# Optimization experiments

Measured on AMD Instinct MI355X. Metric: run time of the kernel, lower is better.

## Reference

```python
import jax, jax.numpy as jnp
import numpy as np
from jax import lax

# Constants matching PostProcess(conf_thres=0.4, iou_thres=0.5, merge=False, agnostic=False)
CONF_THRES = 0.4
IOU_THRES = 0.5
MAX_WH = 4096.0   # per-class box offset (agnostic=False)
MAX_DET = 300     # hardcoded in module
MAX_NMS = 30000   # cap on NMS candidates (yolov5 convention); JAX needs static shapes
B, N, NC = 16, 25200, 80


def setup_inputs() -> dict:
    key = jax.random.key(0)
    u = jax.random.uniform(key, (B, N, 5 + NC), dtype=jnp.float32)
    # cx,cy in [0,640); w,h in [2,102); obj and class scores in [0,1)
    scale = jnp.concatenate([jnp.array([640.0, 640.0, 100.0, 100.0], jnp.float32),
                             jnp.ones((1 + NC,), jnp.float32)])
    shift = jnp.concatenate([jnp.array([0.0, 0.0, 2.0, 2.0], jnp.float32),
                             jnp.zeros((1 + NC,), jnp.float32)])
    prediction = u * scale + shift
    return {"prediction": prediction}


def _cxcywh_to_xyxy(x):
    cx, cy, w, h = x[..., 0], x[..., 1], x[..., 2], x[..., 3]
    return jnp.stack([cx - 0.5 * w, cy - 0.5 * h, cx + 0.5 * w, cy + 0.5 * h], axis=-1)


def _process_one(x):  # x: [N, 5+NC]
    obj = x[:, 4]
    cls_conf = x[:, 5:] * obj[:, None]          # x[:,5:] *= x[:,4:5]
    box = _cxcywh_to_xyxy(x[:, :4])             # [N, 4]
    # multi-label candidate mask: obj > conf AND class conf > conf (x[xc] then x[:,5:] > conf)
    cand = (obj[:, None] > CONF_THRES) & (cls_conf > CONF_THRES)   # [N, NC]
    flat = jnp.where(cand, cls_conf, 0.0).reshape(-1)              # [N*NC]
    top_scores, top_idx = lax.top_k(flat, MAX_NMS)                 # static-size candidate set
    bi = top_idx // NC                                             # box index i
    cj = (top_idx % NC).astype(jnp.float32)                        # class index j
    cand_boxes = box[bi]                                           # [M, 4]
    scores0 = jnp.where(top_scores > CONF_THRES, top_scores, 0.0)  # 0 marks invalid/suppressed
    off_boxes = cand_boxes + cj[:, None] * MAX_WH                  # per-class offset for NMS
    areas = (off_boxes[:, 2] - off_boxes[:, 0]) * (off_boxes[:, 3] - off_boxes[:, 1])
    idx_range = jnp.arange(MAX_NMS)

    def step(scores, _):
        # greedy NMS: pick best remaining, suppress IoU > thresh (torchvision semantics)
        idx = jnp.argmax(scores)
        s = scores[idx]
        keep = s > 0.0
        b = off_boxes[idx]
        lt = jnp.maximum(b[:2], off_boxes[:, :2])
        rb = jnp.minimum(b[2:], off_boxes[:, 2:])
        wh = jnp.clip(rb - lt, 0.0)
        inter = wh[:, 0] * wh[:, 1]
        iou = inter / (areas[idx] + areas - inter + 1e-9)
        suppress = (iou > IOU_THRES) | (idx_range == idx)
        return jnp.where(suppress, 0.0, scores), (idx, keep)

    _, (keep_idx, keep_flag) = lax.scan(step, scores0, None, length=MAX_DET)
    rows = jnp.concatenate([cand_boxes[keep_idx],
                            top_scores[keep_idx][:, None],
                            cj[keep_idx][:, None]], axis=1)        # [MAX_DET, 6] = xyxy, conf, cls
    return jnp.where(keep_flag[:, None], rows, 0.0)


def reference(prediction):
    # Padded fixed-shape analogue of torch.stack(output): [B, MAX_DET, 6], zero rows = no detection
    return jax.vmap(_process_one)(prediction)
```

## Files before the change

### kernel.cpp

```cpp
#include <hip/hip_runtime.h>
#include <stdint.h>

#define BATCH 16
#define NROW 25200
#define NCLS 80
#define ROWF 85
#define MAXDET 300
#define MAXNMS 30000u
#define NBIN 3072
#define BASEBITS 0x3EC00000u
#define CAP 32768u
#define BATCH_FLOATS 2142000

#define PREBIN 2048
#define NBUCK 1024
#define CANDCAP 131072u
#define KMAX 2048u

#define GATHER_MIN 512u
#define SORTCAP 1024
#define CH_SZ 128

#define TILE_ROWS 80
#define TILE_FLOATS 6800
#define RPB 400
#define SUBT 5
#define SBLK 63

#define ROWS_PER_BLK 256
#define SBLK2 99

__device__ __forceinline__ bool iou_gt_half(float ax1, float ay1, float ax2, float ay2, float aa,
                                            float bx1, float by1, float bx2, float by2, float ba) {
    float ltx = fmaxf(ax1, bx1), lty = fmaxf(ay1, by1);
    float rbx = fminf(ax2, bx2), rby = fminf(ay2, by2);
    float wx = fmaxf(__fsub_rn(rbx, ltx), 0.0f);
    float wy = fmaxf(__fsub_rn(rby, lty), 0.0f);
    float inter = __fmul_rn(wx, wy);
    float den = __fadd_rn(__fsub_rn(__fadd_rn(aa, ba), inter), 1e-9f);
    float t = __fmul_rn(0.5f, den);
    if (!(inter > t)) return false;
    float tg = __fmul_rn(0.50000012f, den);
    if (inter >= tg) return true;
    return __fdiv_rn(inter, den) > 0.5f;
}

__device__ __forceinline__ unsigned bin_of_bits(unsigned bits) {
    unsigned v = (bits - BASEBITS) >> 12;
    if (v > (unsigned)(NBIN - 1)) v = NBIN - 1;
    return v;
}

__global__ __launch_bounds__(256) void k_stage(const float* __restrict__ pred,
                                               unsigned* __restrict__ ghist,
                                               unsigned* __restrict__ ccnt,
                                               unsigned long long* __restrict__ cand,
                                               unsigned* __restrict__ oflow,
                                               int staged) {
    if (!staged) return;
    __shared__ unsigned shist[NBUCK];
    __shared__ unsigned long long skey[KMAX];
    __shared__ unsigned s_cnt, s_n, s_base;
    int bx = blockIdx.x;
    int b = bx / SBLK2, blk = bx - b * SBLK2;
    int t = threadIdx.x, lane = t & 63, wv = t >> 6;
    for (int i = t; i < NBUCK; i += 256) shist[i] = 0u;
    if (t == 0) s_cnt = 0u;
    __syncthreads();
    const float* pb = pred + (size_t)b * BATCH_FLOATS;
    int r0 = blk * ROWS_PER_BLK + wv * 64;
    int rown = NROW - r0;
    if (rown > 0) {
        if (rown > 64) rown = 64;
        float obj = 0.0f;
        if (lane < rown) obj = pb[(size_t)(r0 + lane) * ROWF + 4];
        unsigned long long live = __ballot(obj > 0.4f);
        while (live) {
            int j = (int)__builtin_ctzll(live);
            live &= live - 1ULL;
            float o = __shfl(obj, j);
            const float* rp = pb + (size_t)(r0 + j) * ROWF;
            unsigned grow = (unsigned)(r0 + j);
            {
                float s = __fmul_rn(rp[5 + lane], o);
                if (s >= 0.75f) {
                    unsigned bits = __float_as_uint(s);
                    unsigned bin = bin_of_bits(bits);
                    atomicAdd(&shist[bin - PREBIN], 1u);
                    unsigned u = atomicAdd(&s_cnt, 1u);
                    unsigned flat = grow * (unsigned)NCLS + (unsigned)lane;
                    if (u < KMAX)
                        skey[u] = ((unsigned long long)bits << 32) |
                                  (unsigned long long)(0xFFFFFFFFu - flat);
                    else oflow[b] = 1u;
                }
            }
            if (lane < 16) {
                int c = 64 + lane;
                float s = __fmul_rn(rp[5 + c], o);
                if (s >= 0.75f) {
                    unsigned bits = __float_as_uint(s);
                    unsigned bin = bin_of_bits(bits);
                    atomicAdd(&shist[bin - PREBIN], 1u);
                    unsigned u = atomicAdd(&s_cnt, 1u);
                    unsigned flat = grow * (unsigned)NCLS + (unsigned)c;
                    if (u < KMAX)
                        skey[u] = ((unsigned long long)bits << 32) |
                                  (unsigned long long)(0xFFFFFFFFu - flat);
                    else oflow[b] = 1u;
                }
            }
        }
    }
    __syncthreads();
    unsigned* gh = ghist + (size_t)(b * SBLK2 + blk) * NBUCK;
    for (int i = t; i < NBUCK; i += 256) gh[i] = shist[i];
    if (t == 0) {
        unsigned n = s_cnt;
        if (n > KMAX) n = KMAX;
        unsigned base = atomicAdd(&ccnt[b], n);
        if (base + n > CANDCAP) oflow[b] = 1u;
        s_n = n; s_base = base;
    }
    __syncthreads();
    unsigned n = s_n, base = s_base;
    if (base + n <= CANDCAP) {
        unsigned long long* cd = cand + (size_t)b * CANDCAP + base;
        for (unsigned k = t; k < n; k += 256) cd[k] = skey[k];
    }
}

__global__ __launch_bounds__(256) void k_prep(const unsigned* __restrict__ ghist,
                                              const unsigned* __restrict__ ccnt,
                                              const unsigned* __restrict__ oflow,
                                              unsigned* __restrict__ suf2,
                                              int* __restrict__ meta,
                                              int staged) {
    __shared__ unsigned sh[NBUCK];
    __shared__ unsigned sS[NBUCK];
    __shared__ unsigned cs[256];
    __shared__ int s_cut, s_need, s_tot;
    __shared__ unsigned s_bad;
    int b = blockIdx.x, t = threadIdx.x;
    for (int i = t; i < NBUCK; i += 256) {
        unsigned s = 0;
        const unsigned* g = ghist + (size_t)b * SBLK2 * NBUCK + i;
        for (int k = 0; k < SBLK2; ++k) s += g[(size_t)k * NBUCK];
        sh[i] = s;
    }
    if (t == 0) { s_cut = -1; s_need = 0; s_tot = 0; s_bad = 0u; }
    __syncthreads();
    for (int i = t; i < NBUCK; i += 256)
        if (sh[i] > (unsigned)SORTCAP) atomicOr(&s_bad, 1u);
    const int CHUNK = NBUCK / 256;
    int base = t * CHUNK;
    unsigned tot = 0;
    for (int i = 0; i < CHUNK; ++i) tot += sh[base + i];
    cs[t] = tot;
    __syncthreads();
    for (int off = 1; off < 256; off <<= 1) {
        unsigned v = (t + off < 256) ? cs[t + off] : 0u;
        __syncthreads();
        cs[t] += v;
        __syncthreads();
    }
    unsigned after = (t + 1 < 256) ? cs[t + 1] : 0u;
    for (int i = CHUNK - 1; i >= 0; --i) {
        after += sh[base + i];
        sS[base + i] = after;
    }
    __syncthreads();
    unsigned* g2 = suf2 + (size_t)b * (NBUCK + 1);
    for (int i = t; i < NBUCK; i += 256) g2[i] = sS[i];
    if (t == 0) g2[NBUCK] = 0u;
    for (int i = 0; i < CHUNK; ++i) {
        int v = base + i;
        unsigned Sv = sS[v];
        unsigned Sn = (v + 1 < NBUCK) ? sS[v + 1] : 0u;
        if (Sv >= MAXNMS && Sn < MAXNMS) {
            s_cut = PREBIN + v;
            s_need = (int)(MAXNMS - Sn);
            s_tot = (int)Sv;
        }
    }
    __syncthreads();
    if (t == 0) {
        int valid = (staged && s_cut >= 0 && s_bad == 0u &&
                     oflow[b] == 0u && ccnt[b] <= CANDCAP) ? 1 : 0;
        meta[b * 4 + 0] = valid ? s_cut : 0;
        meta[b * 4 + 1] = valid ? s_need : 0;
        meta[b * 4 + 2] = valid ? s_tot : 0;
        meta[b * 4 + 3] = valid;
    }
}

__global__ __launch_bounds__(256) void k_hist_fb(const float* __restrict__ pred,
                                                 unsigned* __restrict__ hist,
                                                 const int* __restrict__ meta) {
    int bx = blockIdx.x;
    int b = bx / SBLK, blk = bx - b * SBLK;
    if (meta[b * 4 + 3]) return;
    __shared__ __align__(16) float rows[TILE_FLOATS];
    __shared__ unsigned shist[NBIN];
    int t = threadIdx.x, lane = t & 63, wv = t >> 6;
    for (int i = t; i < NBIN; i += 256) shist[i] = 0u;
    const float* pbase = pred + (size_t)b * BATCH_FLOATS + (size_t)blk * RPB * ROWF;
    for (int st = 0; st < SUBT; ++st) {
        __syncthreads();
        const float4* src = (const float4*)(pbase + (size_t)st * TILE_ROWS * ROWF);
        float4* dst = (float4*)rows;
        for (int i = t; i < TILE_FLOATS / 4; i += 256) dst[i] = src[i];
        __syncthreads();
        for (int r = wv; r < TILE_ROWS; r += 4) {
            float obj = rows[r * ROWF + 4];
            if (!(obj > 0.4f)) continue;
            for (int half = 0; half < 2; ++half) {
                int c = lane + (half << 6);
                if (c < NCLS) {
                    float cv = rows[r * ROWF + 5 + c];
                    float s = __fmul_rn(cv, obj);
                    if (s > 0.4f) atomicAdd(&shist[bin_of_bits(__float_as_uint(s))], 1u);
                }
            }
        }
    }
    __syncthreads();
    unsigned* gh = hist + (size_t)b * NBIN;
    for (int i = t; i < NBIN; i += 256) {
        unsigned v = shist[i];
        if (v) atomicAdd(&gh[i], v);
    }
}

__global__ __launch_bounds__(256) void k_scan_fb(const unsigned* __restrict__ hist,
                                                 unsigned* __restrict__ suf,
                                                 int* __restrict__ meta) {
    int b = blockIdx.x, t = threadIdx.x;
    if (meta[b * 4 + 3]) return;
    __shared__ unsigned sh[NBIN];
    __shared__ unsigned sS[NBIN];
    __shared__ unsigned cs[256];
    __shared__ int s_cut, s_need, s_tot;
    const unsigned* gh = hist + (size_t)b * NBIN;
    for (int i = t; i < NBIN; i += 256) sh[i] = gh[i];
    if (t == 0) { s_cut = 0; s_need = 0x7FFFFFFF; s_tot = 0; }
    __syncthreads();
    const int CHUNK = NBIN / 256;
    int base = t * CHUNK;
    unsigned tot = 0;
    for (int i = 0; i < CHUNK; ++i) tot += sh[base + i];
    cs[t] = tot;
    __syncthreads();
    for (int off = 1; off < 256; off <<= 1) {
        unsigned v = (t + off < 256) ? cs[t + off] : 0u;
        __syncthreads();
        cs[t] += v;
        __syncthreads();
    }
    unsigned after = (t + 1 < 256) ? cs[t + 1] : 0u;
    for (int i = CHUNK - 1; i >= 0; --i) {
        after += sh[base + i];
        sS[base + i] = after;
    }
    __syncthreads();
    unsigned* gs = suf + (size_t)b * (NBIN + 1);
    for (int i = t; i < NBIN; i += 256) gs[i] = sS[i];
    if (t == 0) gs[NBIN] = 0u;
    for (int i = 0; i < CHUNK; ++i) {
        int v = base + i;
        unsigned Sv = sS[v];
        unsigned Sn = (v + 1 < NBIN) ? sS[v + 1] : 0u;
        if (Sv >= MAXNMS && Sn < MAXNMS) {
            s_cut = v;
            s_need = (int)(MAXNMS - Sn);
            s_tot = (int)Sv;
        }
    }
    __syncthreads();
    if (t == 0) {
        int cut = s_cut, needv = s_need, totv = s_tot;
        if (sS[0] < MAXNMS) { cut = 0; needv = 0x7FFFFFFF; totv = (int)sS[0]; }
        meta[b * 4 + 0] = cut;
        meta[b * 4 + 1] = needv;
        meta[b * 4 + 2] = totv;
    }
}

__global__ __launch_bounds__(256) void k_scatter_fb(const float* __restrict__ pred,
                                                    const unsigned* __restrict__ suf,
                                                    const int* __restrict__ meta,
                                                    unsigned* __restrict__ cursor,
                                                    unsigned long long* __restrict__ keys) {
    int bx = blockIdx.x;
    int b = bx / SBLK, blk = bx - b * SBLK;
    if (meta[b * 4 + 3]) return;
    __shared__ __align__(16) float rows[TILE_FLOATS];
    int t = threadIdx.x, lane = t & 63, wv = t >> 6;
    int cutbin = meta[b * 4 + 0];
    const float* pbase = pred + (size_t)b * BATCH_FLOATS + (size_t)blk * RPB * ROWF;
    unsigned rowbase0 = (unsigned)(blk * RPB);
    const unsigned* gs = suf + (size_t)b * (NBIN + 1);
    unsigned* cur = cursor + (size_t)b * NBIN;
    unsigned long long* kb = keys + (size_t)b * CAP;
    for (int st = 0; st < SUBT; ++st) {
        __syncthreads();
        const float4* src = (const float4*)(pbase + (size_t)st * TILE_ROWS * ROWF);
        float4* dst = (float4*)rows;
        for (int i = t; i < TILE_FLOATS / 4; i += 256) dst[i] = src[i];
        __syncthreads();
        for (int r = wv; r < TILE_ROWS; r += 4) {
            float obj = rows[r * ROWF + 4];
            if (!(obj > 0.4f)) continue;
            unsigned grow = rowbase0 + (unsigned)(st * TILE_ROWS + r);
            for (int half = 0; half < 2; ++half) {
                int c = lane + (half << 6);
                if (c < NCLS) {
                    float cv = rows[r * ROWF + 5 + c];
                    float s = __fmul_rn(cv, obj);
                    if (s > 0.4f) {
                        unsigned bits = __float_as_uint(s);
                        unsigned bin = bin_of_bits(bits);
                        if ((int)bin >= cutbin) {
                            unsigned pos = gs[bin + 1] + atomicAdd(&cur[bin], 1u);
                            if (pos < CAP) {
                                unsigned flat = grow * (unsigned)NCLS + (unsigned)c;
                                kb[pos] = ((unsigned long long)bits << 32) |
                                          (unsigned long long)(0xFFFFFFFFu - flat);
                            }
                        }
                    }
                }
            }
        }
    }
}

__global__ __launch_bounds__(1024) void k_nms(const float* __restrict__ pred,
                                              const unsigned* __restrict__ suf,
                                              const unsigned* __restrict__ suf2,
                                              const int* __restrict__ meta,
                                              const unsigned* __restrict__ ccnt,
                                              const unsigned long long* __restrict__ keys,
                                              const unsigned long long* __restrict__ cand,
                                              float* __restrict__ out) {
    __shared__ unsigned sgsL[NBUCK + 1];
    __shared__ unsigned long long ktmp[SORTCAP];
    __shared__ unsigned long long skeys[SORTCAP];
    __shared__ unsigned maskW[CH_SZ][5];
    __shared__ unsigned sup0w[4];
    __shared__ float cbox[CH_SZ][9];
    __shared__ float kept[MAXDET][5];
    __shared__ int klist[MAXDET];
    __shared__ int s_nk, s_localk;
    __shared__ unsigned s_gc;

    int b = blockIdx.x;
    int tid = threadIdx.x;
    int lane = tid & 63, wv = tid >> 6;

    int cutbin = meta[b * 4 + 0];
    int needv  = meta[b * 4 + 1];
    unsigned total = (unsigned)meta[b * 4 + 2];
    int valid  = meta[b * 4 + 3];
    if (!valid && total > CAP) total = CAP;
    const unsigned* gs = suf + (size_t)b * (NBIN + 1);
    const unsigned* g2 = suf2 + (size_t)b * (NBUCK + 1);
    const unsigned long long* kb = keys + (size_t)b * CAP;
    const unsigned long long* cd = cand + (size_t)b * CANDCAP;
    unsigned ccb = valid ? ccnt[b] : 0u;
    if (ccb > CANDCAP) ccb = CANDCAP;
    const float* pb = pred + (size_t)b * BATCH_FLOATS;
    float* ob = out + (size_t)b * MAXDET * 6;

    if (valid) for (int i = tid; i < NBUCK + 1; i += 1024) sgsL[i] = g2[i];
    if (tid == 0) s_nk = 0;
    __syncthreads();

#define GSV(v) (valid ? sgsL[(v) - PREBIN] : gs[(v)])

    unsigned limit;
    if (needv == 0x7FFFFFFF) limit = total;
    else limit = GSV(cutbin + 1) + (unsigned)needv;
    if (limit > total) limit = total;

    unsigned p = 0;
    while (p < limit) {
        if (s_nk >= MAXDET) break;

        int lo = cutbin, hi = NBIN - 1, w1 = cutbin;
        while (lo <= hi) { int mid = (lo + hi) >> 1;
            if (GSV(mid) > p) { w1 = mid; lo = mid + 1; } else hi = mid - 1; }
        lo = cutbin; hi = NBIN - 1; int w2 = cutbin;
        while (lo <= hi) { int mid = (lo + hi) >> 1;
            if (GSV(mid) >= p + GATHER_MIN) { w2 = mid; lo = mid + 1; } else hi = mid - 1; }
        unsigned gEnd = GSV(w2);
        if (gEnd <= p) gEnd = GSV(cutbin);
        if (gEnd - p > (unsigned)SORTCAP) {
            if (w2 < w1) gEnd = GSV(w2 + 1);
            if (gEnd - p > (unsigned)SORTCAP) gEnd = p + SORTCAP;
        }
        unsigned G = gEnd - p;

        if (valid) {
            if (tid == 0) s_gc = 0u;
            __syncthreads();
            for (unsigned k = tid; k < ccb; k += 1024) {
                unsigned long long key = cd[k];
                unsigned v = bin_of_bits((unsigned)(key >> 32));
                if ((int)v >= w2 && (int)v <= w1) {
                    unsigned u = atomicAdd(&s_gc, 1u);
                    if (u < (unsigned)SORTCAP) ktmp[u] = key;
                }
            }
            __syncthreads();
            unsigned Gc = s_gc; if (Gc > (unsigned)SORTCAP) Gc = (unsigned)SORTCAP;
            if (tid < (int)Gc) {
                unsigned long long key = ktmp[tid];
                unsigned v = bin_of_bits((unsigned)(key >> 32));
                unsigned bstart = GSV(v + 1);
                unsigned rank = 0;
                for (unsigned u = 0; u < Gc; ++u) {
                    unsigned long long kk = ktmp[u];
                    unsigned vu = bin_of_bits((unsigned)(kk >> 32));
                    rank += (vu == v && kk > key) ? 1u : 0u;
                }
                skeys[(bstart - p) + rank] = key;
            }
            __syncthreads();
        } else {
            unsigned myLo = 0, myHi = 0;
            unsigned long long raw = 0ULL;
            if (tid < (int)G) {
                unsigned idx = p + (unsigned)tid;
                int l2 = cutbin, h2 = NBIN - 1, v = cutbin;
                while (l2 <= h2) { int mid = (l2 + h2) >> 1;
                    if (GSV(mid) > idx) { v = mid; l2 = mid + 1; } else h2 = mid - 1; }
                unsigned bstart = GSV(v + 1);
                unsigned bend = GSV(v);
                raw = kb[idx];
                myLo = bstart - p;
                myHi = bend - p; if (myHi > G) myHi = G;
                ktmp[tid] = raw;
            }
            __syncthreads();
            if (tid < (int)G) {
                unsigned rank = 0;
                for (unsigned u = myLo; u < myHi; ++u) rank += (ktmp[u] > raw) ? 1u : 0u;
                skeys[myLo + rank] = raw;
            }
            __syncthreads();
        }

        unsigned consumable = limit - p; if (consumable > G) consumable = G;

        for (unsigned c0 = 0; c0 < consumable; c0 += CH_SZ) {
            int nk0 = s_nk;
            if (nk0 >= MAXDET) break;
            int CH = (int)((consumable - c0 < (unsigned)CH_SZ) ? (consumable - c0) : (unsigned)CH_SZ);

            if (tid < CH_SZ * 5) maskW[tid / 5][tid % 5] = 0u;
            if (tid >= CH_SZ * 5 && tid < CH_SZ * 5 + 4) sup0w[tid - CH_SZ * 5] = 0u;
            if (tid < CH) {
                unsigned long long kk = skeys[c0 + tid];
                unsigned flat = 0xFFFFFFFFu - (unsigned)kk;
                unsigned bi = flat / (unsigned)NCLS;
                unsigned cc = flat - bi * (unsigned)NCLS;
                const float* rp = pb + (size_t)bi * ROWF;
                float cx = rp[0], cy = rp[1], wd = rp[2], ht = rp[3];
                float hw = __fmul_rn(0.5f, wd), hh = __fmul_rn(0.5f, ht);
                float off = __fmul_rn((float)cc, 4096.0f);
                float x1 = __fsub_rn(cx, hw), y1 = __fsub_rn(cy, hh);
                float x2 = __fadd_rn(cx, hw), y2 = __fadd_rn(cy, hh);
                float ox1 = __fadd_rn(x1, off), oy1 = __fadd_rn(y1, off);
                float ox2 = __fadd_rn(x2, off), oy2 = __fadd_rn(y2, off);
                cbox[tid][0] = ox1; cbox[tid][1] = oy1;
                cbox[tid][2] = ox2; cbox[tid][3] = oy2;
                cbox[tid][4] = __fmul_rn(__fsub_rn(ox2, ox1), __fsub_rn(oy2, oy1));
            }
            __syncthreads();

            {
                int col = tid & (CH_SZ - 1);
                int part = tid >> 7;
                if (col < CH) {
                    float bx1 = cbox[col][0], by1 = cbox[col][1];
                    float bx2 = cbox[col][2], by2 = cbox[col][3], ba = cbox[col][4];
                    unsigned part16 = 0u;
                    int rbase = part << 4;
                    for (int k = 0; k < 16; ++k) {
                        int i2 = rbase + k;
                        if (i2 >= col || i2 >= CH) break;
                        if (iou_gt_half(cbox[i2][0], cbox[i2][1], cbox[i2][2], cbox[i2][3],
                                        cbox[i2][4], bx1, by1, bx2, by2, ba))
                            part16 |= (1u << k);
                    }
                    if (part16)
                        atomicOr(&maskW[col][part >> 1], part16 << ((part & 1) << 4));
                    bool f = false;
                    for (int k2 = part; k2 < nk0; k2 += 8) {
                        if (iou_gt_half(kept[k2][0], kept[k2][1], kept[k2][2], kept[k2][3],
                                        kept[k2][4], bx1, by1, bx2, by2, ba)) f = true;
                    }
                    if (f) atomicOr(&sup0w[col >> 5], 1u << (col & 31));
                }
            }
            __syncthreads();

            if (wv == 0) {
                unsigned keptw = 0u;
                int nkv = nk0, lk = 0;
                unsigned pre0 = (lane < 4 && CH > 0) ? maskW[0][lane] : 0u;
                unsigned pre1 = (lane < 4 && CH > 1) ? maskW[1][lane] : 0u;
                for (int j = 0; j < CH && nkv < MAXDET; ++j) {
                    unsigned colw = pre0;
                    pre0 = pre1;
                    pre1 = (lane < 4 && (j + 2) < CH) ? maskW[j + 2][lane] : 0u;
                    bool hit = (keptw & colw) != 0u;
                    bool sup = __any(hit);
                    if ((sup0w[j >> 5] >> (j & 31)) & 1u) sup = true;
                    if (!sup) {
                        if (lane == (j >> 5)) keptw |= 1u << (j & 31);
                        if (lane == 0) klist[lk] = j;
                        lk++; nkv++;
                    }
                }
                if (lane == 0) { s_localk = lk; s_nk = nkv; }
            }
            __syncthreads();

            int lk = s_localk;
            for (int t2 = tid; t2 < lk; t2 += 1024) {
                int i = klist[t2];
                int oidx = nk0 + t2;
                kept[oidx][0] = cbox[i][0]; kept[oidx][1] = cbox[i][1];
                kept[oidx][2] = cbox[i][2]; kept[oidx][3] = cbox[i][3];
                kept[oidx][4] = cbox[i][4];
                unsigned long long kk = skeys[c0 + i];
                unsigned bits = (unsigned)(kk >> 32);
                unsigned flat = 0xFFFFFFFFu - (unsigned)kk;
                unsigned bi = flat / (unsigned)NCLS;
                unsigned cc = flat - bi * (unsigned)NCLS;
                const float* rp = pb + (size_t)bi * ROWF;
                float cx = rp[0], cy = rp[1], wd = rp[2], ht = rp[3];
                float hw = __fmul_rn(0.5f, wd), hh = __fmul_rn(0.5f, ht);
                float* orow = ob + (size_t)oidx * 6;
                orow[0] = __fsub_rn(cx, hw);
                orow[1] = __fsub_rn(cy, hh);
                orow[2] = __fadd_rn(cx, hw);
                orow[3] = __fadd_rn(cy, hh);
                orow[4] = __uint_as_float(bits);
                orow[5] = (float)cc;
            }
            __syncthreads();
        }
        p = gEnd;
    }
#undef GSV
}

extern "C" void kernel_launch(void* const* d_in, const int* in_sizes, int n_in,
                              void* d_out, int out_size, void* d_ws, size_t ws_size,
                              hipStream_t stream) {
    const float* pred = (const float*)d_in[0];
    float* outp = (float*)d_out;
    char* ws = (char*)d_ws;

    const size_t OFF_HIST = 0;
    const size_t SZ_HIST  = (size_t)BATCH * NBIN * 4;
    const size_t OFF_CUR  = OFF_HIST + SZ_HIST;
    const size_t SZ_CUR   = (size_t)BATCH * NBIN * 4;
    const size_t OFF_CCNT = OFF_CUR + SZ_CUR;
    const size_t SZ_CCNT  = (size_t)BATCH * 4;
    const size_t OFF_OFLW = OFF_CCNT + SZ_CCNT;
    const size_t SZ_OFLW  = (size_t)BATCH * 4;
    const size_t OFF_META = OFF_OFLW + SZ_OFLW;
    const size_t SZ_META  = (size_t)BATCH * 4 * 4;
    const size_t ZERO_SZ  = OFF_META + SZ_META;
    const size_t OFF_SUF  = ZERO_SZ;
    const size_t SZ_SUF   = (size_t)BATCH * (NBIN + 1) * 4;
    const size_t OFF_SUF2 = OFF_SUF + SZ_SUF;
    const size_t SZ_SUF2  = (size_t)BATCH * (NBUCK + 1) * 4;
    const size_t OFF_KEYS = OFF_SUF2 + SZ_SUF2;
    const size_t SZ_KEYS  = (size_t)BATCH * CAP * 8;
    const size_t OFF_GH   = OFF_KEYS + SZ_KEYS;
    const size_t SZ_GH    = (size_t)BATCH * SBLK2 * NBUCK * 4;
    const size_t OFF_CAND = OFF_GH + SZ_GH;
    const size_t SZ_CAND  = (size_t)BATCH * CANDCAP * 8;
    const size_t WS_NEEDED = OFF_CAND + SZ_CAND;

    int staged = (ws_size >= WS_NEEDED) ? 1 : 0;

    unsigned* hist             = (unsigned*)(ws + OFF_HIST);
    unsigned* cursor           = (unsigned*)(ws + OFF_CUR);
    unsigned* ccnt             = (unsigned*)(ws + OFF_CCNT);
    unsigned* oflow            = (unsigned*)(ws + OFF_OFLW);
    int* meta                  = (int*)(ws + OFF_META);
    unsigned* suf              = (unsigned*)(ws + OFF_SUF);
    unsigned* suf2             = (unsigned*)(ws + OFF_SUF2);
    unsigned long long* keys   = (unsigned long long*)(ws + OFF_KEYS);
    unsigned* ghist            = (unsigned*)(ws + OFF_GH);
    unsigned long long* cand   = (unsigned long long*)(ws + OFF_CAND);

    hipMemsetAsync(ws, 0, ZERO_SZ, stream);
    hipMemsetAsync(d_out, 0, (size_t)out_size * sizeof(float), stream);

    k_stage<<<dim3(BATCH * SBLK2), dim3(256), 0, stream>>>(pred, ghist, ccnt, cand, oflow, staged);
    k_prep<<<dim3(BATCH), dim3(256), 0, stream>>>(ghist, ccnt, oflow, suf2, meta, staged);
    k_hist_fb<<<dim3(BATCH * SBLK), dim3(256), 0, stream>>>(pred, hist, meta);
    k_scan_fb<<<dim3(BATCH), dim3(256), 0, stream>>>(hist, suf, meta);
    k_scatter_fb<<<dim3(BATCH * SBLK), dim3(256), 0, stream>>>(pred, suf, meta, cursor, keys);
    k_nms<<<dim3(BATCH), dim3(1024), 0, stream>>>(pred, suf, suf2, meta, ccnt, keys, cand, outp);
}
```

Measured before the change: 375.2 us.

## Pre-scatter top candidates into bucket-sorted buffer in prep kernel

The per-block histogram write is replaced by global atomic accumulation into one histogram per batch. The prep kernel now runs with 1024 threads, scans that histogram directly, finds a threshold bin covering the top 2048 candidates, and counting-scatters those candidates into a bucket-ordered keys2 buffer. The NMS kernel then reads its first phase from keys2 with in-bucket rank sorting, so it no longer rescans the whole candidate list for every gather chunk. The costs are global atomics in k_stage and a serial-per-batch scatter pass in k_prep.

```diff
diff --git a/kernel.cpp b/kernel.cpp
--- a/kernel.cpp
+++ b/kernel.cpp
@@ -16,8 +16,9 @@
 #define NBUCK 1024
 #define CANDCAP 131072u
 #define KMAX 2048u
-
-#define GATHER_MIN 512u
+#define TOPK 2048u
+#define K2CAP 4096u
+
 #define SORTCAP 1024
 #define CH_SZ 128
 
@@ -52,7 +53,7 @@
 }
 
 __global__ __launch_bounds__(256) void k_stage(const float* __restrict__ pred,
-                                               unsigned* __restrict__ ghist,
+                                               unsigned* __restrict__ hist2,
                                                unsigned* __restrict__ ccnt,
                                                unsigned long long* __restrict__ cand,
                                                unsigned* __restrict__ oflow,
@@ -113,8 +114,11 @@
         }
     }
     __syncthreads();
-    unsigned* gh = ghist + (size_t)(b * SBLK2 + blk) * NBUCK;
-    for (int i = t; i < NBUCK; i += 256) gh[i] = shist[i];
+    unsigned* gh = hist2 + (size_t)b * NBUCK;
+    for (int i = t; i < NBUCK; i += 256) {
+        unsigned v = shist[i];
+        if (v) atomicAdd(&gh[i], v);
+    }
     if (t == 0) {
         unsigned n = s_cnt;
         if (n > KMAX) n = KMAX;
@@ -130,67 +134,66 @@
     }
 }
 
-__global__ __launch_bounds__(256) void k_prep(const unsigned* __restrict__ ghist,
-                                              const unsigned* __restrict__ ccnt,
-                                              const unsigned* __restrict__ oflow,
-                                              unsigned* __restrict__ suf2,
-                                              int* __restrict__ meta,
-                                              int staged) {
-    __shared__ unsigned sh[NBUCK];
+__global__ __launch_bounds__(1024) void k_prep(const unsigned* __restrict__ hist2,
+                                               const unsigned* __restrict__ ccnt,
+                                               const unsigned* __restrict__ oflow,
+                                               const unsigned long long* __restrict__ cand,
+                                               unsigned* __restrict__ suf2,
+                                               unsigned long long* __restrict__ keys2,
+                                               int* __restrict__ meta,
+                                               int staged) {
     __shared__ unsigned sS[NBUCK];
-    __shared__ unsigned cs[256];
-    __shared__ int s_cut, s_need, s_tot;
-    __shared__ unsigned s_bad;
+    __shared__ unsigned scur[NBUCK];
+    __shared__ int s_cut, s_need, s_tot, s_T, s_valid;
+    __shared__ unsigned s_bad, s_E;
     int b = blockIdx.x, t = threadIdx.x;
-    for (int i = t; i < NBUCK; i += 256) {
-        unsigned s = 0;
-        const unsigned* g = ghist + (size_t)b * SBLK2 * NBUCK + i;
-        for (int k = 0; k < SBLK2; ++k) s += g[(size_t)k * NBUCK];
-        sh[i] = s;
-    }
-    if (t == 0) { s_cut = -1; s_need = 0; s_tot = 0; s_bad = 0u; }
-    __syncthreads();
-    for (int i = t; i < NBUCK; i += 256)
-        if (sh[i] > (unsigned)SORTCAP) atomicOr(&s_bad, 1u);
-    const int CHUNK = NBUCK / 256;
-    int base = t * CHUNK;
-    unsigned tot = 0;
-    for (int i = 0; i < CHUNK; ++i) tot += sh[base + i];
-    cs[t] = tot;
-    __syncthreads();
-    for (int off = 1; off < 256; off <<= 1) {
-        unsigned v = (t + off < 256) ? cs[t + off] : 0u;
-        __syncthreads();
-        cs[t] += v;
-        __syncthreads();
-    }
-    unsigned after = (t + 1 < 256) ? cs[t + 1] : 0u;
-    for (int i = CHUNK - 1; i >= 0; --i) {
-        after += sh[base + i];
-        sS[base + i] = after;
-    }
-    __syncthreads();
+    unsigned h = hist2[(size_t)b * NBUCK + t];
+    sS[t] = h;
+    if (t == 0) { s_cut = -1; s_T = -1; s_bad = 0u; s_need = 0; s_tot = 0; s_E = 0u; }
+    __syncthreads();
+    if (h > (unsigned)SORTCAP) atomicOr(&s_bad, 1u);
+    for (int off = 1; off < NBUCK; off <<= 1) {
+        unsigned v = (t + off < NBUCK) ? sS[t + off] : 0u;
+        __syncthreads();
+        sS[t] += v;
+        __syncthreads();
+    }
+    unsigned Sv = sS[t];
+    unsigned Sn = (t + 1 < NBUCK) ? sS[t + 1] : 0u;
+    if (Sv >= MAXNMS && Sn < MAXNMS) {
+        s_cut = PREBIN + t; s_need = (int)(MAXNMS - Sn); s_tot = (int)Sv;
+    }
+    if (Sv >= TOPK && Sn < TOPK) { s_T = PREBIN + t; s_E = Sv; }
     unsigned* g2 = suf2 + (size_t)b * (NBUCK + 1);
-    for (int i = t; i < NBUCK; i += 256) g2[i] = sS[i];
+    g2[t] = Sv;
     if (t == 0) g2[NBUCK] = 0u;
-    for (int i = 0; i < CHUNK; ++i) {
-        int v = base + i;
-        unsigned Sv = sS[v];
-        unsigned Sn = (v + 1 < NBUCK) ? sS[v + 1] : 0u;
-        if (Sv >= MAXNMS && Sn < MAXNMS) {
-            s_cut = PREBIN + v;
-            s_need = (int)(MAXNMS - Sn);
-            s_tot = (int)Sv;
+    scur[t] = Sn;
+    __syncthreads();
+    if (t == 0) {
+        int valid = (staged && s_cut >= 0 && s_T >= 0 && s_bad == 0u &&
+                     oflow[b] == 0u && ccnt[b] <= CANDCAP) ? 1 : 0;
+        s_valid = valid;
+        meta[b * 8 + 0] = valid ? s_cut : 0;
+        meta[b * 8 + 1] = valid ? s_need : 0;
+        meta[b * 8 + 2] = valid ? s_tot : 0;
+        meta[b * 8 + 3] = valid;
+        meta[b * 8 + 4] = valid ? s_T : 0;
+        meta[b * 8 + 5] = valid ? (int)s_E : 0;
+    }
+    __syncthreads();
+    if (s_valid) {
+        int T = s_T;
+        unsigned ccb = ccnt[b];
+        const unsigned long long* cd = cand + (size_t)b * CANDCAP;
+        unsigned long long* k2 = keys2 + (size_t)b * K2CAP;
+        for (unsigned k = t; k < ccb; k += 1024) {
+            unsigned long long key = cd[k];
+            unsigned v = bin_of_bits((unsigned)(key >> 32));
+            if ((int)v >= T) {
+                unsigned pos = atomicAdd(&scur[v - PREBIN], 1u);
+                if (pos < K2CAP) k2[pos] = key;
+            }
         }
-    }
-    __syncthreads();
-    if (t == 0) {
-        int valid = (staged && s_cut >= 0 && s_bad == 0u &&
-                     oflow[b] == 0u && ccnt[b] <= CANDCAP) ? 1 : 0;
-        meta[b * 4 + 0] = valid ? s_cut : 0;
-        meta[b * 4 + 1] = valid ? s_need : 0;
-        meta[b * 4 + 2] = valid ? s_tot : 0;
-        meta[b * 4 + 3] = valid;
     }
 }
 
@@ -199,7 +202,7 @@
                                                  const int* __restrict__ meta) {
     int bx = blockIdx.x;
     int b = bx / SBLK, blk = bx - b * SBLK;
-    if (meta[b * 4 + 3]) return;
+    if (meta[b * 8 + 3]) return;
     __shared__ __align__(16) float rows[TILE_FLOATS];
     __shared__ unsigned shist[NBIN];
     int t = threadIdx.x, lane = t & 63, wv = t >> 6;
@@ -217,8 +220,7 @@
             for (int half = 0; half < 2; ++half) {
                 int c = lane + (half << 6);
                 if (c < NCLS) {
-                    float cv = rows[r * ROWF + 5 + c];
-                    float s = __fmul_rn(cv, obj);
+                    float s = __fmul_rn(rows[r * ROWF + 5 + c], obj);
                     if (s > 0.4f) atomicAdd(&shist[bin_of_bits(__float_as_uint(s))], 1u);
                 }
             }
@@ -236,7 +238,7 @@
                                                  unsigned* __restrict__ suf,
                                                  int* __restrict__ meta) {
     int b = blockIdx.x, t = threadIdx.x;
-    if (meta[b * 4 + 3]) return;
+    if (meta[b * 8 + 3]) return;
     __shared__ unsigned sh[NBIN];
     __shared__ unsigned sS[NBIN];
     __shared__ unsigned cs[256];
@@ -271,18 +273,16 @@
         unsigned Sv = sS[v];
         unsigned Sn = (v + 1 < NBIN) ? sS[v + 1] : 0u;
         if (Sv >= MAXNMS && Sn < MAXNMS) {
-            s_cut = v;
-            s_need = (int)(MAXNMS - Sn);
-            s_tot = (int)Sv;
+            s_cut = v; s_need = (int)(MAXNMS - Sn); s_tot = (int)Sv;
         }
     }
     __syncthreads();
     if (t == 0) {
         int cut = s_cut, needv = s_need, totv = s_tot;
         if (sS[0] < MAXNMS) { cut = 0; needv = 0x7FFFFFFF; totv = (int)sS[0]; }
-        meta[b * 4 + 0] = cut;
-        meta[b * 4 + 1] = needv;
-        meta[b * 4 + 2] = totv;
+        meta[b * 8 + 0] = cut;
+        meta[b * 8 + 1] = needv;
+        meta[b * 8 + 2] = totv;
     }
 }
 
@@ -293,10 +293,10 @@
                                                     unsigned long long* __restrict__ keys) {
     int bx = blockIdx.x;
     int b = bx / SBLK, blk = bx - b * SBLK;
-    if (meta[b * 4 + 3]) return;
+    if (meta[b * 8 + 3]) return;
     __shared__ __align__(16) float rows[TILE_FLOATS];
     int t = threadIdx.x, lane = t & 63, wv = t >> 6;
-    int cutbin = meta[b * 4 + 0];
+    int cutbin = meta[b * 8 + 0];
     const float* pbase = pred + (size_t)b * BATCH_FLOATS + (size_t)blk * RPB * ROWF;
     unsigned rowbase0 = (unsigned)(blk * RPB);
     const unsigned* gs = suf + (size_t)b * (NBIN + 1);
@@ -315,8 +315,7 @@
             for (int half = 0; half < 2; ++half) {
                 int c = lane + (half << 6);
                 if (c < NCLS) {
-                    float cv = rows[r * ROWF + 5 + c];
-                    float s = __fmul_rn(cv, obj);
+                    float s = __fmul_rn(rows[r * ROWF + 5 + c], obj);
                     if (s > 0.4f) {
                         unsigned bits = __float_as_uint(s);
                         unsigned bin = bin_of_bits(bits);
@@ -341,6 +340,7 @@
                                               const int* __restrict__ meta,
                                               const unsigned* __restrict__ ccnt,
                                               const unsigned long long* __restrict__ keys,
+                                              const unsigned long long* __restrict__ keys2,
                                               const unsigned long long* __restrict__ cand,
                                               float* __restrict__ out) {
     __shared__ unsigned sgsL[NBUCK + 1];
@@ -358,14 +358,17 @@
     int tid = threadIdx.x;
     int lane = tid & 63, wv = tid >> 6;
 
-    int cutbin = meta[b * 4 + 0];
-    int needv  = meta[b * 4 + 1];
-    unsigned total = (unsigned)meta[b * 4 + 2];
-    int valid  = meta[b * 4 + 3];
+    int cutbin = meta[b * 8 + 0];
+    int needv  = meta[b * 8 + 1];
+    unsigned total = (unsigned)meta[b * 8 + 2];
+    int valid  = meta[b * 8 + 3];
+    int Tbin   = meta[b * 8 + 4];
+    unsigned E = valid ? (unsigned)meta[b * 8 + 5] : 0u;
     if (!valid && total > CAP) total = CAP;
     const unsigned* gs = suf + (size_t)b * (NBIN + 1);
     const unsigned* g2 = suf2 + (size_t)b * (NBUCK + 1);
     const unsigned long long* kb = keys + (size_t)b * CAP;
+    const unsigned long long* k2 = keys2 + (size_t)b * K2CAP;
     const unsigned long long* cd = cand + (size_t)b * CANDCAP;
     unsigned ccb = valid ? ccnt[b] : 0u;
     if (ccb > CANDCAP) ccb = CANDCAP;
@@ -387,27 +390,49 @@
     while (p < limit) {
         if (s_nk >= MAXDET) break;
 
-        int lo = cutbin, hi = NBIN - 1, w1 = cutbin;
+        int lo = cutbin, hi = NBIN - 1, vs = NBIN - 1;
         while (lo <= hi) { int mid = (lo + hi) >> 1;
-            if (GSV(mid) > p) { w1 = mid; lo = mid + 1; } else hi = mid - 1; }
-        lo = cutbin; hi = NBIN - 1; int w2 = cutbin;
-        while (lo <= hi) { int mid = (lo + hi) >> 1;
-            if (GSV(mid) >= p + GATHER_MIN) { w2 = mid; lo = mid + 1; } else hi = mid - 1; }
-        unsigned gEnd = GSV(w2);
-        if (gEnd <= p) gEnd = GSV(cutbin);
-        if (gEnd - p > (unsigned)SORTCAP) {
-            if (w2 < w1) gEnd = GSV(w2 + 1);
-            if (gEnd - p > (unsigned)SORTCAP) gEnd = p + SORTCAP;
-        }
+            if (GSV(mid) <= p + (unsigned)SORTCAP) { vs = mid; hi = mid - 1; } else lo = mid + 1; }
+        unsigned gEnd = GSV(vs);
+        bool phaseA = (!valid) || (p < E);
+        if (valid && phaseA && gEnd > E) gEnd = E;
+        if (gEnd > total) gEnd = total;
+        if (gEnd <= p) { gEnd = p + (unsigned)SORTCAP; if (gEnd > total) gEnd = total; }
         unsigned G = gEnd - p;
 
-        if (valid) {
+        if (phaseA) {
+            const unsigned long long* src = valid ? k2 : kb;
+            unsigned myLo = 0, myHi = 0;
+            unsigned long long raw = 0ULL;
+            if (tid < (int)G) {
+                unsigned idx = p + (unsigned)tid;
+                int l2 = cutbin, h2 = NBIN - 1, v = cutbin;
+                while (l2 <= h2) { int mid = (l2 + h2) >> 1;
+                    if (GSV(mid) > idx) { v = mid; l2 = mid + 1; } else h2 = mid - 1; }
+                unsigned bstart = GSV(v + 1);
+                unsigned bend = GSV(v);
+                raw = src[idx];
+                myLo = (bstart > p) ? (bstart - p) : 0u;
+                myHi = bend - p; if (myHi > G) myHi = G;
+                ktmp[tid] = raw;
+            }
+            __syncthreads();
+            if (tid < (int)G) {
+                unsigned rank = 0;
+                for (unsigned u = myLo; u < myHi; ++u) rank += (ktmp[u] > raw) ? 1u : 0u;
+                skeys[myLo + rank] = raw;
+            }
+            __syncthreads();
+        } else {
+            int l0 = cutbin, h0 = NBIN - 1, w1 = cutbin;
+            while (l0 <= h0) { int mid = (l0 + h0) >> 1;
+                if (GSV(mid) > p) { w1 = mid; l0 = mid + 1; } else h0 = mid - 1; }
             if (tid == 0) s_gc = 0u;
             __syncthreads();
             for (unsigned k = tid; k < ccb; k += 1024) {
                 unsigned long long key = cd[k];
                 unsigned v = bin_of_bits((unsigned)(key >> 32));
-                if ((int)v >= w2 && (int)v <= w1) {
+                if ((int)v >= vs && (int)v <= w1) {
                     unsigned u = atomicAdd(&s_gc, 1u);
                     if (u < (unsigned)SORTCAP) ktmp[u] = key;
                 }
@@ -425,28 +450,6 @@
                     rank += (vu == v && kk > key) ? 1u : 0u;
                 }
                 skeys[(bstart - p) + rank] = key;
-            }
-            __syncthreads();
-        } else {
-            unsigned myLo = 0, myHi = 0;
-            unsigned long long raw = 0ULL;
-            if (tid < (int)G) {
-                unsigned idx = p + (unsigned)tid;
-                int l2 = cutbin, h2 = NBIN - 1, v = cutbin;
-                while (l2 <= h2) { int mid = (l2 + h2) >> 1;
-                    if (GSV(mid) > idx) { v = mid; l2 = mid + 1; } else h2 = mid - 1; }
-                unsigned bstart = GSV(v + 1);
-                unsigned bend = GSV(v);
-                raw = kb[idx];
-                myLo = bstart - p;
-                myHi = bend - p; if (myHi > G) myHi = G;
-                ktmp[tid] = raw;
-            }
-            __syncthreads();
-            if (tid < (int)G) {
-                unsigned rank = 0;
-                for (unsigned u = myLo; u < myHi; ++u) rank += (ktmp[u] > raw) ? 1u : 0u;
-                skeys[myLo + rank] = raw;
             }
             __syncthreads();
         }
@@ -565,49 +568,52 @@
     float* outp = (float*)d_out;
     char* ws = (char*)d_ws;
 
-    const size_t OFF_HIST = 0;
-    const size_t SZ_HIST  = (size_t)BATCH * NBIN * 4;
-    const size_t OFF_CUR  = OFF_HIST + SZ_HIST;
-    const size_t SZ_CUR   = (size_t)BATCH * NBIN * 4;
-    const size_t OFF_CCNT = OFF_CUR + SZ_CUR;
-    const size_t SZ_CCNT  = (size_t)BATCH * 4;
-    const size_t OFF_OFLW = OFF_CCNT + SZ_CCNT;
-    const size_t SZ_OFLW  = (size_t)BATCH * 4;
-    const size_t OFF_META = OFF_OFLW + SZ_OFLW;
-    const size_t SZ_META  = (size_t)BATCH * 4 * 4;
-    const size_t ZERO_SZ  = OFF_META + SZ_META;
-    const size_t OFF_SUF  = ZERO_SZ;
-    const size_t SZ_SUF   = (size_t)BATCH * (NBIN + 1) * 4;
-    const size_t OFF_SUF2 = OFF_SUF + SZ_SUF;
-    const size_t SZ_SUF2  = (size_t)BATCH * (NBUCK + 1) * 4;
-    const size_t OFF_KEYS = OFF_SUF2 + SZ_SUF2;
-    const size_t SZ_KEYS  = (size_t)BATCH * CAP * 8;
-    const size_t OFF_GH   = OFF_KEYS + SZ_KEYS;
-    const size_t SZ_GH    = (size_t)BATCH * SBLK2 * NBUCK * 4;
-    const size_t OFF_CAND = OFF_GH + SZ_GH;
-    const size_t SZ_CAND  = (size_t)BATCH * CANDCAP * 8;
+    const size_t OFF_HIST  = 0;
+    const size_t SZ_HIST   = (size_t)BATCH * NBIN * 4;
+    const size_t OFF_CUR   = OFF_HIST + SZ_HIST;
+    const size_t SZ_CUR    = (size_t)BATCH * NBIN * 4;
+    const size_t OFF_H2    = OFF_CUR + SZ_CUR;
+    const size_t SZ_H2     = (size_t)BATCH * NBUCK * 4;
+    const size_t OFF_CCNT  = OFF_H2 + SZ_H2;
+    const size_t SZ_CCNT   = (size_t)BATCH * 4;
+    const size_t OFF_OFLW  = OFF_CCNT + SZ_CCNT;
+    const size_t SZ_OFLW   = (size_t)BATCH * 4;
+    const size_t OFF_META  = OFF_OFLW + SZ_OFLW;
+    const size_t SZ_META   = (size_t)BATCH * 8 * 4;
+    const size_t ZERO_SZ   = OFF_META + SZ_META;
+    const size_t OFF_SUF   = ZERO_SZ;
+    const size_t SZ_SUF    = (size_t)BATCH * (NBIN + 1) * 4;
+    const size_t OFF_SUF2  = OFF_SUF + SZ_SUF;
+    const size_t SZ_SUF2   = (size_t)BATCH * (NBUCK + 1) * 4;
+    const size_t OFF_KEYS  = OFF_SUF2 + SZ_SUF2;
+    const size_t SZ_KEYS   = (size_t)BATCH * CAP * 8;
+    const size_t OFF_K2    = OFF_KEYS + SZ_KEYS;
+    const size_t SZ_K2     = (size_t)BATCH * K2CAP * 8;
+    const size_t OFF_CAND  = OFF_K2 + SZ_K2;
+    const size_t SZ_CAND   = (size_t)BATCH * CANDCAP * 8;
     const size_t WS_NEEDED = OFF_CAND + SZ_CAND;
 
     int staged = (ws_size >= WS_NEEDED) ? 1 : 0;
 
     unsigned* hist             = (unsigned*)(ws + OFF_HIST);
     unsigned* cursor           = (unsigned*)(ws + OFF_CUR);
+    unsigned* hist2            = (unsigned*)(ws + OFF_H2);
     unsigned* ccnt             = (unsigned*)(ws + OFF_CCNT);
     unsigned* oflow            = (unsigned*)(ws + OFF_OFLW);
     int* meta                  = (int*)(ws + OFF_META);
     unsigned* suf              = (unsigned*)(ws + OFF_SUF);
     unsigned* suf2             = (unsigned*)(ws + OFF_SUF2);
     unsigned long long* keys   = (unsigned long long*)(ws + OFF_KEYS);
-    unsigned* ghist            = (unsigned*)(ws + OFF_GH);
+    unsigned long long* keys2  = (unsigned long long*)(ws + OFF_K2);
     unsigned long long* cand   = (unsigned long long*)(ws + OFF_CAND);
 
     hipMemsetAsync(ws, 0, ZERO_SZ, stream);
     hipMemsetAsync(d_out, 0, (size_t)out_size * sizeof(float), stream);
 
-    k_stage<<<dim3(BATCH * SBLK2), dim3(256), 0, stream>>>(pred, ghist, ccnt, cand, oflow, staged);
-    k_prep<<<dim3(BATCH), dim3(256), 0, stream>>>(ghist, ccnt, oflow, suf2, meta, staged);
+    k_stage<<<dim3(BATCH * SBLK2), dim3(256), 0, stream>>>(pred, hist2, ccnt, cand, oflow, staged);
+    k_prep<<<dim3(BATCH), dim3(1024), 0, stream>>>(hist2, ccnt, oflow, cand, suf2, keys2, meta, staged);
     k_hist_fb<<<dim3(BATCH * SBLK), dim3(256), 0, stream>>>(pred, hist, meta);
     k_scan_fb<<<dim3(BATCH), dim3(256), 0, stream>>>(hist, suf, meta);
     k_scatter_fb<<<dim3(BATCH * SBLK), dim3(256), 0, stream>>>(pred, suf, meta, cursor, keys);
-    k_nms<<<dim3(BATCH), dim3(1024), 0, stream>>>(pred, suf, suf2, meta, ccnt, keys, cand, outp);
-}
+    k_nms<<<dim3(BATCH), dim3(1024), 0, stream>>>(pred, suf, suf2, meta, ccnt, keys, keys2, cand, outp);
+}
```

Result: faster. 347.7 us (-7.3%).
